# Kernel tuning notes

Hardware: AMD Instinct MI355X
Metric: run time of the kernel (lower is better)

The kernel has to match this reference:

```python
import jax, jax.numpy as jnp
import numpy as np

K = 8          # branching factor
D = 4          # tree depth (leaves at depth D)
H = 32         # const node dim
LEAVES = K ** D  # 4096
B = 32
OUT = 2
EPS = 1e-5


def _layer_dims(d):
    # depth d layer: in = (#units at depth d+1), out = (#nodes at d) * H
    n = K ** d
    in_per_child = H if d < D - 1 else 1  # leaf layer feeds scalars
    return n, n * K * in_per_child, n * H, in_per_child


def setup_inputs() -> dict:
    key = jax.random.key(0)
    ks = jax.random.split(key, 64)
    inp = {"x": jax.random.normal(ks[0], (B, LEAVES), jnp.float32)}
    i = 1
    for d in range(D - 1, -1, -1):
        n, fin, fout, ipc = _layer_dims(d)
        # block-diagonal pruning mask: node j rows <- its K children's blocks
        mask = jnp.asarray(np.kron(np.eye(n, dtype=np.float32),
                                   np.ones((H, K * ipc), dtype=np.float32)))
        s = 1.0 / np.sqrt(fin)
        inp[f"Wm{d}"] = jax.random.uniform(ks[i], (fout, fin), jnp.float32, -s, s) * mask; i += 1
        inp[f"bm{d}"] = jax.random.uniform(ks[i], (fout,), jnp.float32, -s, s); i += 1
        inp[f"Wl{d}"] = jax.random.uniform(ks[i], (fout, fin), jnp.float32, -s, s) * mask; i += 1
        inp[f"bl{d}"] = jax.random.uniform(ks[i], (fout,), jnp.float32, -s, s); i += 1
    inp["gate"] = jnp.float32(0.3)
    inp["bn_gamma"] = jnp.ones((H,), jnp.float32)
    inp["bn_beta"] = jnp.zeros((H,), jnp.float32)
    so = 1.0 / np.sqrt(H)
    inp["Wout"] = jax.random.uniform(ks[i], (OUT, H), jnp.float32, -so, so); i += 1
    inp["bout"] = jax.random.uniform(ks[i], (OUT,), jnp.float32, -so, so)
    return inp


def reference(x, Wm3, bm3, Wl3, bl3, Wm2, bm2, Wl2, bl2,
              Wm1, bm1, Wl1, bl1, Wm0, bm0, Wl0, bl0,
              gate, bn_gamma, bn_beta, Wout, bout):
    x_linear = x
    layers = ((Wm3, bm3, Wl3, bl3), (Wm2, bm2, Wl2, bl2),
              (Wm1, bm1, Wl1, bl1), (Wm0, bm0, Wl0, bl0))
    for Wm, bm, Wl, bl in layers:  # depth D-1 -> 0, as in torch forward
        h = jax.nn.relu(x @ Wm.T + bm)          # mlp branch (masked weights)
        x_linear = x_linear @ Wl.T + bl          # parallel linear branch
        x = h * gate + (1.0 - gate) * x_linear   # gated residual combine
    # BatchNorm1d in training mode (biased batch variance)
    mu = jnp.mean(x, axis=0)
    var = jnp.var(x, axis=0)
    xn = (x - mu) * jax.lax.rsqrt(var + EPS)
    y = xn * bn_gamma + bn_beta
    return y @ Wout.T + bout
```

## Files before the change

### kernel.cpp

```cpp
#include <hip/hip_runtime.h>


#define MAGIC 0x5CA1AB1E

__device__ __forceinline__ float dot4(float4 a, float4 b, float acc) {
    acc = fmaf(a.x, b.x, acc);
    acc = fmaf(a.y, b.y, acc);
    acc = fmaf(a.z, b.z, acc);
    acc = fmaf(a.w, b.w, acc);
    return acc;
}
__device__ __forceinline__ float4 ld4(const float* p) { return *(const float4*)p; }

typedef const __attribute__((address_space(1))) void* gas_t;
typedef __attribute__((address_space(3))) void* las_t;

__device__ __forceinline__ void gl_lds16(const float* g, float* l) {
    __builtin_amdgcn_global_load_lds((gas_t)g, (las_t)l, 16, 0, 0);
}
__device__ __forceinline__ void gl_lds4(const float* g, float* l) {
    __builtin_amdgcn_global_load_lds((gas_t)g, (las_t)l, 4, 0, 0);
}
__device__ __forceinline__ void st_xch(float* p, float v) { (void)atomicExch(p, v); }
__device__ __forceinline__ float ld_wt(const float* p) {
    return __int_as_float(
        __hip_atomic_load((const int*)p, __ATOMIC_RELAXED, __HIP_MEMORY_SCOPE_AGENT));
}
__device__ __forceinline__ void flag_set(int* p) {
    __atomic_signal_fence(__ATOMIC_SEQ_CST);
    __hip_atomic_store(p, MAGIC, __ATOMIC_RELAXED, __HIP_MEMORY_SCOPE_AGENT);
}
__device__ __forceinline__ void flag_wait(const int* p) {
    while (__hip_atomic_load(p, __ATOMIC_RELAXED, __HIP_MEMORY_SCOPE_AGENT) != MAGIC)
        __builtin_amdgcn_s_sleep(1);
    __atomic_signal_fence(__ATOMIC_SEQ_CST);
}

__global__ __launch_bounds__(512)
void fused_tree(const float* __restrict__ x,
                const float* __restrict__ Wm3, const float* __restrict__ bm3,
                const float* __restrict__ Wl3, const float* __restrict__ bl3,
                const float* __restrict__ Wm2, const float* __restrict__ bm2,
                const float* __restrict__ Wl2, const float* __restrict__ bl2,
                const float* __restrict__ Wm1, const float* __restrict__ bm1,
                const float* __restrict__ Wl1, const float* __restrict__ bl1,
                const float* __restrict__ Wm0, const float* __restrict__ bm0,
                const float* __restrict__ Wl0, const float* __restrict__ bl0,
                const float* __restrict__ gate_p,
                const float* __restrict__ bn_gamma, const float* __restrict__ bn_beta,
                const float* __restrict__ Wout, const float* __restrict__ bout,
                float* __restrict__ Qm, float* __restrict__ Ql,
                float* __restrict__ Pm, float* __restrict__ Pl,
                int* __restrict__ flags1, int* __restrict__ flags2,
                float* __restrict__ out)
{
    const int blk = blockIdx.x;
    const int j2 = blk & 63, rg = blk >> 6;
    const int tid = threadIdx.x;
    const int wv = tid >> 6, ln = tid & 63;
    const int j1 = j2 >> 3, s = j2 & 7;
    const int cid = rg * 8 + j1;
    const bool is_consumer = (s == 0);

    __shared__ __align__(16) float xs[8][64];
    __shared__ __align__(16) float w2[2][32][260];
    __shared__ __align__(16) float w1s[2][32][32];
    __shared__ __align__(16) float x3[8][260];
    __shared__ __align__(16) float xl3[8][260];
    __shared__ __align__(16) float x2s[8][36];
    __shared__ __align__(16) float xl2s[8][36];
    __shared__ __align__(16) float x1s[8][36];
    __shared__ __align__(16) float xl1s[8][36];
    __shared__ float x0s[32][33];
    __shared__ float bnm[32], bna[32];
    __shared__ float pW[64], pbo[2], pg[32], pb[32], pbm0[32], pbl0[32];

    gl_lds4(x + (rg * 8 + wv) * 4096 + j2 * 64 + ln, &xs[wv][0]);
#pragma unroll
    for (int i = 0; i < 8; ++i) {
        const int q = wv * 8 + i;
        const int m = q >> 5, r = q & 31;
        const float* src = (m ? Wl2 : Wm2)
                         + (size_t)(j2 * 32 + r) * 16384 + j2 * 256 + ln * 4;
        gl_lds16(src, &w2[m][r][0]);
    }
    {
        const int m1 = wv >> 2, r0 = (wv & 3) * 8;
        const int r = r0 + (ln >> 3), c = (ln & 7) * 4;
        const float* W1 = m1 ? Wl1 : Wm1;
        gl_lds16(W1 + (size_t)(j1 * 32 + r) * 2048 + j2 * 32 + c, &w1s[m1][r0][0]);
    }

    const int col = tid & 255, hh3 = tid >> 8;
    const int l3 = col >> 5, t3 = col & 31;
    const int j3 = j2 * 8 + l3;
    const int row3 = j3 * 32 + t3;
    const float* wmr = Wm3 + (size_t)row3 * 4096 + j3 * 8;
    const float* wlr = Wl3 + (size_t)row3 * 4096 + j3 * 8;
    const float4 wma = ld4(wmr), wmb = ld4(wmr + 4);
    const float4 wla = ld4(wlr), wlb = ld4(wlr + 4);
    const float bm3v = bm3[row3], bl3v = bl3[row3];
    const int t2 = tid >> 4;
    const float bm2v = bm2[j2 * 32 + t2];
    const float bl2v = bl2[j2 * 32 + t2];
    const float g = gate_p[0], gi = 1.0f - g;

    float4 wm0r[8], wl0r[8];
    float bm1v = 0.0f, bl1v = 0.0f;
    if (is_consumer && tid < 256) {
        const int o = tid & 31;
        const float* p0 = Wm0 + o * 256 + j1 * 32;
        const float* p1 = Wl0 + o * 256 + j1 * 32;
#pragma unroll
        for (int k = 0; k < 8; ++k) {
            wm0r[k] = ld4(p0 + k * 4);
            wl0r[k] = ld4(p1 + k * 4);
        }
        bm1v = bm1[j1 * 32 + o];
        bl1v = bl1[j1 * 32 + o];
    }
    if (blk == 0) {
        if (tid < 64) pW[tid] = Wout[tid];
        if (tid < 32) {
            pg[tid]   = bn_gamma[tid];
            pb[tid]   = bn_beta[tid];
            pbm0[tid] = bm0[tid];
            pbl0[tid] = bl0[tid];
        }
        if (tid < 2) pbo[tid] = bout[tid];
    }

    __syncthreads();

#pragma unroll
    for (int i = 0; i < 4; ++i) {
        const int b = hh3 * 4 + i;
        const float4 xa = ld4(&xs[b][l3 * 8]);
        const float4 xb = ld4(&xs[b][l3 * 8 + 4]);
        float am = dot4(xa, wma, bm3v); am = dot4(xb, wmb, am);
        float al = dot4(xa, wla, bl3v); al = dot4(xb, wlb, al);
        x3[b][col]  = fmaf(g, fmaxf(am, 0.0f), gi * al);
        xl3[b][col] = al;
    }
    __syncthreads();

    {
        const int b = (tid >> 1) & 7, hh = tid & 1;
        const float* wmp = &w2[0][t2][hh * 128];
        const float* wlp = &w2[1][t2][hh * 128];
        float pm = 0.0f, pl = 0.0f;
#pragma unroll 8
        for (int c = 0; c < 128; c += 4) {
            pm = dot4(ld4(&x3 [b][hh * 128 + c]), ld4(wmp + c), pm);
            pl = dot4(ld4(&xl3[b][hh * 128 + c]), ld4(wlp + c), pl);
        }
        pm += __shfl_xor(pm, 1);
        pl += __shfl_xor(pl, 1);
        const float am = pm + bm2v, al = pl + bl2v;
        if (hh == 0) x2s [b][t2] = fmaf(g, fmaxf(am, 0.0f), gi * al);
        else         xl2s[b][t2] = al;
    }
    __syncthreads();

    {
        const int t1 = tid >> 4, b = (tid >> 1) & 7, h = tid & 1;
        const float* wm = &w1s[0][t1][h * 16];
        const float* wl = &w1s[1][t1][h * 16];
        const float* xp = &x2s [b][h * 16];
        const float* xq = &xl2s[b][h * 16];
        float pm = 0.0f, pl = 0.0f;
#pragma unroll
        for (int c = 0; c < 16; c += 4) {
            pm = dot4(ld4(xp + c), ld4(wm + c), pm);
            pl = dot4(ld4(xq + c), ld4(wl + c), pl);
        }
        pm += __shfl_xor(pm, 1);
        pl += __shfl_xor(pl, 1);
        const int qi = ((cid * 8 + s) * 8 + b) * 32 + t1;
        if (h == 0) st_xch(&Qm[qi], pm);
        else        st_xch(&Ql[qi], pl);
    }
    __syncthreads();
    if (tid == 0) flag_set(&flags1[cid * 8 + s]);
    if (!is_consumer) return;

    if (tid < 8) flag_wait(&flags1[cid * 8 + tid]);
    __syncthreads();

    if (tid < 256) {
        const int b = tid >> 5, t1 = tid & 31;
        float am = bm1v, al = bl1v;
#pragma unroll
        for (int t = 0; t < 8; ++t) {
            am += ld_wt(&Qm[((cid * 8 + t) * 8 + b) * 32 + t1]);
            al += ld_wt(&Ql[((cid * 8 + t) * 8 + b) * 32 + t1]);
        }
        x1s [b][t1] = fmaf(g, fmaxf(am, 0.0f), gi * al);
        xl1s[b][t1] = al;
    }
    __syncthreads();

    if (tid < 256) {
        const int b = tid >> 5, o = tid & 31;
        float pm0 = 0.0f, pl0 = 0.0f;
#pragma unroll
        for (int k = 0; k < 8; ++k) {
            pm0 = dot4(ld4(&x1s [b][k * 4]), wm0r[k], pm0);
            pl0 = dot4(ld4(&xl1s[b][k * 4]), wl0r[k], pl0);
        }
        const int r = rg * 8 + b;
        st_xch(&Pm[j1 * 1024 + r * 32 + o], pm0);
        st_xch(&Pl[j1 * 1024 + r * 32 + o], pl0);
    }
    __syncthreads();
    if (tid == 0) flag_set(&flags2[cid]);
    if (blk != 0) return;

    if (tid < 31) flag_wait(&flags2[tid + 1]);
    __syncthreads();

    for (int i = tid; i < 1024; i += 512) {
        const int r = i >> 5, o = i & 31;
        float am = pbm0[o], al = pbl0[o];
#pragma unroll
        for (int j = 0; j < 8; ++j) {
            am += ld_wt(&Pm[j * 1024 + r * 32 + o]);
            al += ld_wt(&Pl[j * 1024 + r * 32 + o]);
        }
        x0s[r][o] = fmaf(g, fmaxf(am, 0.0f), gi * al);
    }
    __syncthreads();

    if (tid < 32) {
        float sum = 0.0f, s2 = 0.0f;
#pragma unroll
        for (int r = 0; r < 32; ++r) {
            const float v = x0s[r][tid];
            sum += v;
            s2 = fmaf(v, v, s2);
        }
        const float mu  = sum * (1.0f / 32.0f);
        const float var = s2 * (1.0f / 32.0f) - mu * mu;
        const float m = pg[tid] * rsqrtf(var + 1e-5f);
        bnm[tid] = m;
        bna[tid] = fmaf(-mu, m, pb[tid]);
    }
    __syncthreads();

    if (tid < 64) {
        const int b = tid >> 1, oo = tid & 1;
        float acc = pbo[oo];
#pragma unroll
        for (int t = 0; t < 32; ++t) {
            const float xn = fmaf(x0s[b][t], bnm[t], bna[t]);
            acc = fmaf(xn, pW[oo * 32 + t], acc);
        }
        out[b * 2 + oo] = acc;
    }
}

extern "C" void kernel_launch(void* const* d_in, const int* in_sizes, int n_in,
                              void* d_out, int out_size, void* d_ws, size_t ws_size,
                              hipStream_t stream)
{
    const float* x    = (const float*)d_in[0];
    const float* Wm3  = (const float*)d_in[1];
    const float* bm3  = (const float*)d_in[2];
    const float* Wl3  = (const float*)d_in[3];
    const float* bl3  = (const float*)d_in[4];
    const float* Wm2  = (const float*)d_in[5];
    const float* bm2  = (const float*)d_in[6];
    const float* Wl2  = (const float*)d_in[7];
    const float* bl2  = (const float*)d_in[8];
    const float* Wm1  = (const float*)d_in[9];
    const float* bm1  = (const float*)d_in[10];
    const float* Wl1  = (const float*)d_in[11];
    const float* bl1  = (const float*)d_in[12];
    const float* Wm0  = (const float*)d_in[13];
    const float* bm0  = (const float*)d_in[14];
    const float* Wl0  = (const float*)d_in[15];
    const float* bl0  = (const float*)d_in[16];
    const float* gate = (const float*)d_in[17];
    const float* bn_g = (const float*)d_in[18];
    const float* bn_b = (const float*)d_in[19];
    const float* Wout = (const float*)d_in[20];
    const float* bout = (const float*)d_in[21];
    float* outp = (float*)d_out;

    float* ws     = (float*)d_ws;
    float* Qm     = ws;
    float* Ql     = ws + 65536;
    float* Pm     = ws + 131072;
    float* Pl     = ws + 139264;
    int*   flags1 = (int*)(ws + 147456);
    int*   flags2 = flags1 + 256;

    hipLaunchKernelGGL(fused_tree, dim3(256), dim3(512), 0, stream,
                       x, Wm3, bm3, Wl3, bl3, Wm2, bm2, Wl2, bl2,
                       Wm1, bm1, Wl1, bl1, Wm0, bm0, Wl0, bl0,
                       gate, bn_g, bn_b, Wout, bout,
                       Qm, Ql, Pm, Pl, flags1, flags2, outp);
}
```

Baseline: 18.30 us.

## Load leaf inputs and level-1/0 weights into registers and keep consumer partials local

The leaf inputs x and the level-1 weights are now loaded straight into registers instead of being staged through LDS, which removes the first block-wide barrier before the level-3 compute. The level-0 weight loads are spread across all 512 threads with a shuffle reduction. Consumer blocks keep their own level-1 partial sums in shared memory instead of writing them to global memory and waiting on their own flag. Scheduling barriers are added to order the loads. The cost is higher register pressure in a 512-thread block and more uncoalesced per-thread global loads.

```diff
diff --git a/kernel.cpp b/kernel.cpp
--- a/kernel.cpp
+++ b/kernel.cpp
@@ -17,9 +17,6 @@
 
 __device__ __forceinline__ void gl_lds16(const float* g, float* l) {
     __builtin_amdgcn_global_load_lds((gas_t)g, (las_t)l, 16, 0, 0);
-}
-__device__ __forceinline__ void gl_lds4(const float* g, float* l) {
-    __builtin_amdgcn_global_load_lds((gas_t)g, (las_t)l, 4, 0, 0);
 }
 __device__ __forceinline__ void st_xch(float* p, float v) { (void)atomicExch(p, v); }
 __device__ __forceinline__ float ld_wt(const float* p) {
@@ -62,20 +59,40 @@
     const int cid = rg * 8 + j1;
     const bool is_consumer = (s == 0);
 
-    __shared__ __align__(16) float xs[8][64];
     __shared__ __align__(16) float w2[2][32][260];
-    __shared__ __align__(16) float w1s[2][32][32];
     __shared__ __align__(16) float x3[8][260];
     __shared__ __align__(16) float xl3[8][260];
     __shared__ __align__(16) float x2s[8][36];
     __shared__ __align__(16) float xl2s[8][36];
+    __shared__ __align__(16) float qm_own[8][36];
+    __shared__ __align__(16) float ql_own[8][36];
     __shared__ __align__(16) float x1s[8][36];
     __shared__ __align__(16) float xl1s[8][36];
     __shared__ float x0s[32][33];
     __shared__ float bnm[32], bna[32];
     __shared__ float pW[64], pbo[2], pg[32], pb[32], pbm0[32], pbl0[32];
 
-    gl_lds4(x + (rg * 8 + wv) * 4096 + j2 * 64 + ln, &xs[wv][0]);
+    const int col = tid & 255, hh3 = tid >> 8;
+    const int l3 = col >> 5, t3 = col & 31;
+    const int j3 = j2 * 8 + l3;
+    const int row3 = j3 * 32 + t3;
+
+    float4 xra[4], xrb[4];
+#pragma unroll
+    for (int i = 0; i < 4; ++i) {
+        const float* xp = x + (size_t)(rg * 8 + hh3 * 4 + i) * 4096 + j3 * 8;
+        xra[i] = ld4(xp);
+        xrb[i] = ld4(xp + 4);
+    }
+    const float* wmr = Wm3 + (size_t)row3 * 4096 + j3 * 8;
+    const float* wlr = Wl3 + (size_t)row3 * 4096 + j3 * 8;
+    const float4 wma = ld4(wmr), wmb = ld4(wmr + 4);
+    const float4 wla = ld4(wlr), wlb = ld4(wlr + 4);
+    const float bm3v = bm3[row3], bl3v = bl3[row3];
+    const float g = gate_p[0], gi = 1.0f - g;
+
+    __builtin_amdgcn_sched_barrier(0);
+
 #pragma unroll
     for (int i = 0; i < 8; ++i) {
         const int q = wv * 8 + i;
@@ -84,40 +101,39 @@
                          + (size_t)(j2 * 32 + r) * 16384 + j2 * 256 + ln * 4;
         gl_lds16(src, &w2[m][r][0]);
     }
-    {
-        const int m1 = wv >> 2, r0 = (wv & 3) * 8;
-        const int r = r0 + (ln >> 3), c = (ln & 7) * 4;
-        const float* W1 = m1 ? Wl1 : Wm1;
-        gl_lds16(W1 + (size_t)(j1 * 32 + r) * 2048 + j2 * 32 + c, &w1s[m1][r0][0]);
-    }
-
-    const int col = tid & 255, hh3 = tid >> 8;
-    const int l3 = col >> 5, t3 = col & 31;
-    const int j3 = j2 * 8 + l3;
-    const int row3 = j3 * 32 + t3;
-    const float* wmr = Wm3 + (size_t)row3 * 4096 + j3 * 8;
-    const float* wlr = Wl3 + (size_t)row3 * 4096 + j3 * 8;
-    const float4 wma = ld4(wmr), wmb = ld4(wmr + 4);
-    const float4 wla = ld4(wlr), wlb = ld4(wlr + 4);
-    const float bm3v = bm3[row3], bl3v = bl3[row3];
+    __builtin_amdgcn_sched_barrier(0);
+
     const int t2 = tid >> 4;
     const float bm2v = bm2[j2 * 32 + t2];
     const float bl2v = bl2[j2 * 32 + t2];
-    const float g = gate_p[0], gi = 1.0f - g;
-
-    float4 wm0r[8], wl0r[8];
+
+    const int hp = tid & 1;
+    float4 wm1r[4], wl1r[4];
+    {
+        const float* wr = Wm1 + (size_t)(j1 * 32 + t2) * 2048 + j2 * 32 + hp * 16;
+        const float* lr = Wl1 + (size_t)(j1 * 32 + t2) * 2048 + j2 * 32 + hp * 16;
+#pragma unroll
+        for (int k = 0; k < 4; ++k) {
+            wm1r[k] = ld4(wr + k * 4);
+            wl1r[k] = ld4(lr + k * 4);
+        }
+    }
+
+    float4 wm0r[4], wl0r[4];
     float bm1v = 0.0f, bl1v = 0.0f;
-    if (is_consumer && tid < 256) {
-        const int o = tid & 31;
-        const float* p0 = Wm0 + o * 256 + j1 * 32;
-        const float* p1 = Wl0 + o * 256 + j1 * 32;
-#pragma unroll
-        for (int k = 0; k < 8; ++k) {
+    if (is_consumer) {
+        const int o2 = tid >> 4;
+        const float* p0 = Wm0 + o2 * 256 + j1 * 32 + hp * 16;
+        const float* p1 = Wl0 + o2 * 256 + j1 * 32 + hp * 16;
+#pragma unroll
+        for (int k = 0; k < 4; ++k) {
             wm0r[k] = ld4(p0 + k * 4);
             wl0r[k] = ld4(p1 + k * 4);
         }
-        bm1v = bm1[j1 * 32 + o];
-        bl1v = bl1[j1 * 32 + o];
+        if (tid < 256) {
+            bm1v = bm1[j1 * 32 + (tid & 31)];
+            bl1v = bl1[j1 * 32 + (tid & 31)];
+        }
     }
     if (blk == 0) {
         if (tid < 64) pW[tid] = Wout[tid];
@@ -130,68 +146,70 @@
         if (tid < 2) pbo[tid] = bout[tid];
     }
 
-    __syncthreads();
-
 #pragma unroll
     for (int i = 0; i < 4; ++i) {
         const int b = hh3 * 4 + i;
-        const float4 xa = ld4(&xs[b][l3 * 8]);
-        const float4 xb = ld4(&xs[b][l3 * 8 + 4]);
-        float am = dot4(xa, wma, bm3v); am = dot4(xb, wmb, am);
-        float al = dot4(xa, wla, bl3v); al = dot4(xb, wlb, al);
+        float am = dot4(xra[i], wma, bm3v); am = dot4(xrb[i], wmb, am);
+        float al = dot4(xra[i], wla, bl3v); al = dot4(xrb[i], wlb, al);
         x3[b][col]  = fmaf(g, fmaxf(am, 0.0f), gi * al);
         xl3[b][col] = al;
     }
     __syncthreads();
 
     {
-        const int b = (tid >> 1) & 7, hh = tid & 1;
-        const float* wmp = &w2[0][t2][hh * 128];
-        const float* wlp = &w2[1][t2][hh * 128];
+        const int b = (tid >> 1) & 7;
+        const float* wmp = &w2[0][t2][hp * 128];
+        const float* wlp = &w2[1][t2][hp * 128];
         float pm = 0.0f, pl = 0.0f;
 #pragma unroll 8
         for (int c = 0; c < 128; c += 4) {
-            pm = dot4(ld4(&x3 [b][hh * 128 + c]), ld4(wmp + c), pm);
-            pl = dot4(ld4(&xl3[b][hh * 128 + c]), ld4(wlp + c), pl);
+            pm = dot4(ld4(&x3 [b][hp * 128 + c]), ld4(wmp + c), pm);
+            pl = dot4(ld4(&xl3[b][hp * 128 + c]), ld4(wlp + c), pl);
         }
         pm += __shfl_xor(pm, 1);
         pl += __shfl_xor(pl, 1);
         const float am = pm + bm2v, al = pl + bl2v;
-        if (hh == 0) x2s [b][t2] = fmaf(g, fmaxf(am, 0.0f), gi * al);
+        if (hp == 0) x2s [b][t2] = fmaf(g, fmaxf(am, 0.0f), gi * al);
         else         xl2s[b][t2] = al;
     }
     __syncthreads();
 
     {
-        const int t1 = tid >> 4, b = (tid >> 1) & 7, h = tid & 1;
-        const float* wm = &w1s[0][t1][h * 16];
-        const float* wl = &w1s[1][t1][h * 16];
-        const float* xp = &x2s [b][h * 16];
-        const float* xq = &xl2s[b][h * 16];
+        const int b = (tid >> 1) & 7;
+        const float* xp = &x2s [b][hp * 16];
+        const float* xq = &xl2s[b][hp * 16];
         float pm = 0.0f, pl = 0.0f;
 #pragma unroll
-        for (int c = 0; c < 16; c += 4) {
-            pm = dot4(ld4(xp + c), ld4(wm + c), pm);
-            pl = dot4(ld4(xq + c), ld4(wl + c), pl);
+        for (int k = 0; k < 4; ++k) {
+            pm = dot4(ld4(xp + k * 4), wm1r[k], pm);
+            pl = dot4(ld4(xq + k * 4), wl1r[k], pl);
         }
         pm += __shfl_xor(pm, 1);
         pl += __shfl_xor(pl, 1);
-        const int qi = ((cid * 8 + s) * 8 + b) * 32 + t1;
-        if (h == 0) st_xch(&Qm[qi], pm);
-        else        st_xch(&Ql[qi], pl);
-    }
-    __syncthreads();
-    if (tid == 0) flag_set(&flags1[cid * 8 + s]);
-    if (!is_consumer) return;
-
-    if (tid < 8) flag_wait(&flags1[cid * 8 + tid]);
+        if (is_consumer) {
+            if (hp == 0) qm_own[b][t2] = pm;
+            else         ql_own[b][t2] = pl;
+        } else {
+            const int qi = ((cid * 8 + s) * 8 + b) * 32 + t2;
+            if (hp == 0) st_xch(&Qm[qi], pm);
+            else         st_xch(&Ql[qi], pl);
+        }
+    }
+    __syncthreads();
+    if (!is_consumer) {
+        if (tid == 0) flag_set(&flags1[cid * 8 + s]);
+        return;
+    }
+
+    if (tid < 7) flag_wait(&flags1[cid * 8 + 1 + tid]);
     __syncthreads();
 
     if (tid < 256) {
         const int b = tid >> 5, t1 = tid & 31;
-        float am = bm1v, al = bl1v;
-#pragma unroll
-        for (int t = 0; t < 8; ++t) {
+        float am = bm1v + qm_own[b][t1];
+        float al = bl1v + ql_own[b][t1];
+#pragma unroll
+        for (int t = 1; t < 8; ++t) {
             am += ld_wt(&Qm[((cid * 8 + t) * 8 + b) * 32 + t1]);
             al += ld_wt(&Ql[((cid * 8 + t) * 8 + b) * 32 + t1]);
         }
@@ -200,21 +218,25 @@
     }
     __syncthreads();
 
-    if (tid < 256) {
-        const int b = tid >> 5, o = tid & 31;
+    {
+        const int o2 = tid >> 4, b = (tid >> 1) & 7;
         float pm0 = 0.0f, pl0 = 0.0f;
 #pragma unroll
-        for (int k = 0; k < 8; ++k) {
-            pm0 = dot4(ld4(&x1s [b][k * 4]), wm0r[k], pm0);
-            pl0 = dot4(ld4(&xl1s[b][k * 4]), wl0r[k], pl0);
-        }
+        for (int k = 0; k < 4; ++k) {
+            pm0 = dot4(ld4(&x1s [b][hp * 16 + k * 4]), wm0r[k], pm0);
+            pl0 = dot4(ld4(&xl1s[b][hp * 16 + k * 4]), wl0r[k], pl0);
+        }
+        pm0 += __shfl_xor(pm0, 1);
+        pl0 += __shfl_xor(pl0, 1);
         const int r = rg * 8 + b;
-        st_xch(&Pm[j1 * 1024 + r * 32 + o], pm0);
-        st_xch(&Pl[j1 * 1024 + r * 32 + o], pl0);
-    }
-    __syncthreads();
-    if (tid == 0) flag_set(&flags2[cid]);
-    if (blk != 0) return;
+        if (hp == 0) st_xch(&Pm[j1 * 1024 + r * 32 + o2], pm0);
+        else         st_xch(&Pl[j1 * 1024 + r * 32 + o2], pl0);
+    }
+    __syncthreads();
+    if (blk != 0) {
+        if (tid == 0) flag_set(&flags2[cid]);
+        return;
+    }
 
     if (tid < 31) flag_wait(&flags2[tid + 1]);
     __syncthreads();
```

New measurement: 17.13 us, median of 3. -6.4%, faster.
